# Optimization experiments

Measured on AMD Instinct MI355X. Metric: run time of the kernel, lower is better.

## Reference

```python
import jax, jax.numpy as jnp
import numpy as np

H_SIZE = 1024
N_HEADS = 16
HEAD_DIM = H_SIZE // N_HEADS
TAU2 = 1.0
LN_EPS = 1e-5


def setup_inputs() -> dict:
    key = jax.random.key(0)
    ks = jax.random.split(key, 12)
    B, S = 2, 1024
    s = 1.0 / np.sqrt(H_SIZE)
    inp = {
        "input": jax.random.normal(ks[0], (B, S, H_SIZE), dtype=jnp.float32),
        "input_mask": jnp.ones((B, S), dtype=jnp.float32),
        # uniform(0,1) noise; converted to Gumbel(0,1) inside reference
        "gumbel": jax.random.uniform(ks[1], (B, N_HEADS, S, S), dtype=jnp.float32,
                                     minval=1e-10, maxval=1.0),
        "Wq": jax.random.normal(ks[2], (H_SIZE, H_SIZE), dtype=jnp.float32) * s,
        "bq": jnp.zeros((H_SIZE,), dtype=jnp.float32),
        "Wk": jax.random.normal(ks[3], (H_SIZE, H_SIZE), dtype=jnp.float32) * s,
        "bk": jnp.zeros((H_SIZE,), dtype=jnp.float32),
        "Wv": jax.random.normal(ks[4], (H_SIZE, H_SIZE), dtype=jnp.float32) * s,
        "bv": jnp.zeros((H_SIZE,), dtype=jnp.float32),
        "Wo": jax.random.normal(ks[5], (H_SIZE, H_SIZE), dtype=jnp.float32) * s,
        "bo": jnp.zeros((H_SIZE,), dtype=jnp.float32),
        "gamma": jnp.ones((H_SIZE,), dtype=jnp.float32),
        "beta": jnp.zeros((H_SIZE,), dtype=jnp.float32),
    }
    return inp


def reference(input, input_mask, gumbel, Wq, bq, Wk, bk, Wv, bv, Wo, bo, gamma, beta):
    B, S, _ = input.shape
    # projections -> [B, H, S, D]
    def proj(W, b):
        y = jnp.einsum('bsh,oh->bso', input, W) + b  # torch Linear: x @ W.T + b
        return y.reshape(B, S, N_HEADS, HEAD_DIM).transpose(0, 2, 1, 3)
    qq = proj(Wq, bq)
    kk = proj(Wk, bk)
    vv = proj(Wv, bv)
    # raw scores (NOTE: original has no 1/sqrt(d) scaling)
    interact = jnp.einsum('bhqd,bhkd->bhqk', qq, kk)
    # gumbel-softmax (soft): softmax((logits + g)/tau)
    g = -jnp.log(-jnp.log(gumbel))
    sto_attn = jax.nn.softmax((interact + g) / TAU2, axis=-1)
    # masking: mask_1 over query dim, mask_2 over key dim
    mask = input_mask[:, None, :, None] * input_mask[:, None, None, :]  # [B,1,S,S]
    attn = sto_attn * mask
    # (dropout p=0 -> identity)
    out = jnp.einsum('bhqk,bhkd->bhqd', attn, vv)
    out = out.transpose(0, 2, 1, 3).reshape(B, S, H_SIZE)
    out = jnp.einsum('bsh,oh->bso', out, Wo) + bo
    # residual + layernorm
    x = out + input
    mu = jnp.mean(x, axis=-1, keepdims=True)
    var = jnp.mean(jnp.square(x - mu), axis=-1, keepdims=True)
    return (x - mu) * jax.lax.rsqrt(var + LN_EPS) * gamma + beta
```

## Files before the change

kernel.cpp:

```cpp
#include <hip/hip_runtime.h>

#define S_LEN 1024
#define HSZ   1024
#define NHEAD 16
#define HD    64
#define BATCH 2
#define MROWS 2048
#define SOFTMAX_M0 50.0f

typedef unsigned short u16;
typedef __attribute__((ext_vector_type(8))) short short8;
typedef __attribute__((ext_vector_type(4))) short short4v;
typedef __attribute__((ext_vector_type(4))) float f32x4;

#define MFMA_BF16(a, b, c) __builtin_amdgcn_mfma_f32_16x16x32_bf16((a), (b), (c), 0, 0, 0)

__device__ __forceinline__ u16 f2bf(float f) {
    union { float f; unsigned u; } c; c.f = f;
    unsigned u = c.u;
    u += 0x7fffu + ((u >> 16) & 1u);
    return (u16)(u >> 16);
}
__device__ __forceinline__ float bf2f(u16 s) {
    union { unsigned u; float f; } c; c.u = ((unsigned)s) << 16;
    return c.f;
}
__device__ __forceinline__ short8 ld8(const u16* p) {
    return *reinterpret_cast<const short8*>(p);
}
__device__ __forceinline__ void gld16(const u16* g, u16* l) {
    __builtin_amdgcn_global_load_lds(
        (const __attribute__((address_space(1))) unsigned int*)g,
        (__attribute__((address_space(3))) unsigned int*)l, 16, 0, 0);
}
__device__ __forceinline__ int frag_off(int row, int cbb) {
    return (((row << 3) | (cbb ^ (row & 7))) << 3);
}

template<int MT>
__device__ __forceinline__ void gemm_tile(const u16* __restrict__ Ag,
                                          const u16* __restrict__ Bg,
                                          int klen, u16* As, u16* Bs,
                                          f32x4 (&acc)[MT][4]) {
    const int tid  = threadIdx.x;
    const int wave = tid >> 6, lane = tid & 63;
    const int lr = lane & 15, grp = lane >> 4;
    const int wm = wave >> 1, wn = wave & 1;
    const int ASZ = MT * 2048;
    const int BSZ = 8192;

#pragma unroll
    for (int mt = 0; mt < MT; mt++)
#pragma unroll
        for (int nt = 0; nt < 4; nt++)
            acc[mt][nt] = (f32x4){0.f, 0.f, 0.f, 0.f};

    auto stage = [&](int k0, u16* Ah, u16* Bh) {
#pragma unroll
        for (int j = 0; j < MT; j++) {
            int c = j * 256 + tid, row = c >> 3, cb = (c & 7) ^ (row & 7);
            gld16(Ag + (size_t)row * HSZ + k0 + cb * 8, Ah + c * 8);
        }
#pragma unroll
        for (int j = 0; j < 4; j++) {
            int c = j * 256 + tid, row = c >> 3, cb = (c & 7) ^ (row & 7);
            gld16(Bg + (size_t)row * HSZ + k0 + cb * 8, Bh + c * 8);
        }
    };

    stage(0, As, Bs);

    for (int k0 = 0; k0 < klen; k0 += 64) {
        const int cur = (k0 >> 6) & 1;
        const u16* Ac = As + cur * ASZ;
        const u16* Bc = Bs + cur * BSZ;
        __syncthreads();
        if (k0 + 64 < klen)
            stage(k0 + 64, As + (cur ^ 1) * ASZ, Bs + (cur ^ 1) * BSZ);

#pragma unroll
        for (int h = 0; h < 2; h++) {
            const int cbb = h * 4 + grp;
            short8 af[MT], bf[4];
#pragma unroll
            for (int mt = 0; mt < MT; mt++)
                af[mt] = ld8(Ac + frag_off(wm * (MT * 16) + mt * 16 + lr, cbb));
#pragma unroll
            for (int nt = 0; nt < 4; nt++)
                bf[nt] = ld8(Bc + frag_off(wn * 64 + nt * 16 + lr, cbb));
#pragma unroll
            for (int mt = 0; mt < MT; mt++)
#pragma unroll
                for (int nt = 0; nt < 4; nt++)
                    acc[mt][nt] = MFMA_BF16(af[mt], bf[nt], acc[mt][nt]);
        }
    }
}

__global__ __launch_bounds__(256)
void convert_kernel(const float* __restrict__ x,  const float* __restrict__ wq,
                    const float* __restrict__ wk, const float* __restrict__ wv,
                    const float* __restrict__ wo, u16* __restrict__ dst) {
    const int XV = (MROWS * HSZ) / 4;
    const int WV = (HSZ * HSZ) / 4;
    int vid = blockIdx.x * 256 + threadIdx.x;
    const float* src; int off;
    if (vid < XV)            { src = x;  off = vid; }
    else if (vid < XV + WV)  { src = wq; off = vid - XV; }
    else if (vid < XV + 2*WV){ src = wk; off = vid - XV - WV; }
    else if (vid < XV + 3*WV){ src = wv; off = vid - XV - 2*WV; }
    else                     { src = wo; off = vid - XV - 3*WV; }
    float4 v = reinterpret_cast<const float4*>(src)[off];
    ushort4 o;
    o.x = f2bf(v.x); o.y = f2bf(v.y); o.z = f2bf(v.z); o.w = f2bf(v.w);
    reinterpret_cast<ushort4*>(dst)[vid] = o;
}

__global__ __launch_bounds__(256)
void qkv_gemm(const u16* __restrict__ xb,
              const u16* __restrict__ wqb, const u16* __restrict__ wkb,
              const u16* __restrict__ wvb,
              const float* __restrict__ bq, const float* __restrict__ bk,
              const float* __restrict__ bv, const float* __restrict__ mask,
              u16* __restrict__ qout, u16* __restrict__ kout,
              u16* __restrict__ vtout) {
    __shared__ u16 As[2 * 64 * 64];
    __shared__ u16 Bs[2 * 128 * 64];
    const int ntile = blockIdx.x;
    const int mtile = blockIdx.y;
    const int p  = ntile >> 3;
    const int m0 = mtile * 64;
    const int nw = (ntile & 7) * 128;
    const u16*  W    = (p == 0) ? wqb : (p == 1) ? wkb : wvb;
    const float* bias = (p == 0) ? bq : (p == 1) ? bk : bv;

    f32x4 acc[2][4];
    gemm_tile<2>(xb + (size_t)m0 * HSZ, W + (size_t)nw * HSZ, HSZ, As, Bs, acc);

    const int wave = threadIdx.x >> 6, lane = threadIdx.x & 63;
    const int lr = lane & 15, grp = lane >> 4;
    const int wm = wave >> 1, wn = wave & 1;
#pragma unroll
    for (int mt = 0; mt < 2; mt++)
#pragma unroll
        for (int nt = 0; nt < 4; nt++)
#pragma unroll
            for (int r = 0; r < 4; r++) {
                int m = m0 + wm * 32 + mt * 16 + grp * 4 + r;
                int o = nw + wn * 64 + nt * 16 + lr;
                float val = acc[mt][nt][r] + bias[o];
                int b = m >> 10, s = m & 1023, hh = o >> 6, d = o & 63;
                if (p == 0)
                    qout[(((size_t)(b * NHEAD + hh)) * S_LEN + s) * HD + d] = f2bf(val);
                else if (p == 1)
                    kout[(((size_t)(b * NHEAD + hh)) * S_LEN + s) * HD + d] = f2bf(val);
                else
                    vtout[(((size_t)(b * NHEAD + hh)) * HD + d) * S_LEN + s] =
                        f2bf(val * mask[m]);
            }
}

__global__ __launch_bounds__(256, 4)
void attn_kernel(const u16* __restrict__ qb, const u16* __restrict__ kb,
                 const u16* __restrict__ vt, const float* __restrict__ gumbel,
                 u16* __restrict__ po, float* __restrict__ pl) {
    const int bh   = blockIdx.y;
    const int qt   = blockIdx.x;
    const int half = blockIdx.z;
    const int q0 = qt * 64, kbase = half * 512;
    const int tid = threadIdx.x;
    const int wave = tid >> 6, lane = tid & 63;
    const int lr = lane & 15, grp = lane >> 4;

    const u16* Q = qb + (size_t)bh * S_LEN * HD;
    const u16* K = kb + (size_t)bh * S_LEN * HD;
    const u16* V = vt + (size_t)bh * HD * S_LEN;
    const int qw = q0 + wave * 16;
    const float* Gp = gumbel + (size_t)bh * S_LEN * S_LEN + (size_t)(qw + lr) * S_LEN;

    __shared__ u16 Ks[2][64 * 64];
    __shared__ u16 pbuf[4 * 16 * 68];
    u16* pw = pbuf + wave * (16 * 68);

    short8 aq0 = ld8(Q + (size_t)(qw + lr) * HD + grp * 8);
    short8 aq1 = ld8(Q + (size_t)(qw + lr) * HD + 32 + grp * 8);

    f32x4 acco[4];
#pragma unroll
    for (int i = 0; i < 4; i++) acco[i] = (f32x4){0.f, 0.f, 0.f, 0.f};
    float lsum = 0.f;

    f32x4 gc[4], gn[4];
#pragma unroll
    for (int kt = 0; kt < 4; kt++)
        gc[kt] = *reinterpret_cast<const f32x4*>(Gp + kbase + kt * 16 + grp * 4);

    auto stageK = [&](int k0, u16* Kh) {
#pragma unroll
        for (int j = 0; j < 2; j++) {
            int c = j * 256 + tid, row = c >> 3, cb = (c & 7) ^ (row & 7);
            gld16(K + (size_t)(k0 + row) * HD + cb * 8, Kh + c * 8);
        }
    };
    stageK(kbase, Ks[0]);

#pragma unroll 1
    for (int it = 0; it < 8; it++) {
        const int k0 = kbase + it * 64;
        const int cur = it & 1;

        __syncthreads();
        if (it < 7) {
            stageK(k0 + 64, Ks[cur ^ 1]);
#pragma unroll
            for (int kt = 0; kt < 4; kt++)
                gn[kt] = *reinterpret_cast<const f32x4*>(
                             Gp + k0 + 64 + kt * 16 + grp * 4);
        }

#pragma unroll
        for (int kt = 0; kt < 4; kt++) {
            short8 kf0 = ld8(Ks[cur] + frag_off(kt * 16 + lr, grp));
            short8 kf1 = ld8(Ks[cur] + frag_off(kt * 16 + lr, 4 + grp));
            f32x4 a = (f32x4){0.f, 0.f, 0.f, 0.f};
            a = MFMA_BF16(kf0, aq0, a);
            a = MFMA_BF16(kf1, aq1, a);
            float p[4];
#pragma unroll
            for (int r = 0; r < 4; r++) {
                float w = -__builtin_amdgcn_rcpf(__logf(gc[kt][r]));
                p[r] = __expf(a[r] - SOFTMAX_M0) * w;
                lsum += p[r];
            }
            ushort4 pk;
            pk.x = f2bf(p[0]); pk.y = f2bf(p[1]);
            pk.z = f2bf(p[2]); pk.w = f2bf(p[3]);
            *reinterpret_cast<ushort4*>(pw + lr * 68 + kt * 16 + grp * 4) = pk;
        }

        short8 pa[2];
#pragma unroll
        for (int ks = 0; ks < 2; ks++) {
            const u16* pp = pw + lr * 68 + ks * 32 + grp * 8;
            short4v lo = *reinterpret_cast<const short4v*>(pp);
            short4v hi = *reinterpret_cast<const short4v*>(pp + 4);
            pa[ks] = __builtin_shufflevector(lo, hi, 0, 1, 2, 3, 4, 5, 6, 7);
        }

#pragma unroll
        for (int nt = 0; nt < 4; nt++) {
            const u16* vp = V + (size_t)(nt * 16 + lr) * S_LEN + k0 + grp * 8;
            acco[nt] = MFMA_BF16(pa[0], ld8(vp), acco[nt]);
            acco[nt] = MFMA_BF16(pa[1], ld8(vp + 32), acco[nt]);
        }

        if (it < 7) {
#pragma unroll
            for (int kt = 0; kt < 4; kt++) gc[kt] = gn[kt];
        }
    }

    lsum += __shfl_xor(lsum, 16, 64);
    lsum += __shfl_xor(lsum, 32, 64);

    const int qbase = ((half * 32 + bh) * 16 + qt) * 64 + wave * 16;
    if (lane < 16) pl[qbase + lane] = lsum;

    const int qidx = qbase + grp * 4;
#pragma unroll
    for (int nt = 0; nt < 4; nt++)
#pragma unroll
        for (int r = 0; r < 4; r++)
            po[(size_t)(qidx + r) * 64 + nt * 16 + lr] = f2bf(acco[nt][r]);
}

__global__ __launch_bounds__(256)
void combine_kernel(const u16* __restrict__ po, const float* __restrict__ pl,
                    const float* __restrict__ mask, u16* __restrict__ ctx) {
    const int qt = blockIdx.x, bh = blockIdx.y;
    const int b = bh >> 4, h = bh & 15;
    const int q = threadIdx.x >> 2;
    const int dc = (threadIdx.x & 3) * 16;
    const int i0 = ((0 * 32 + bh) * 16 + qt) * 64 + q;
    const int i1 = ((1 * 32 + bh) * 16 + qt) * 64 + q;
    float l = pl[i0] + pl[i1];
    float mq = mask[b * S_LEN + qt * 64 + q] / l;
    u16* dst = ctx + ((size_t)(b * S_LEN + qt * 64 + q)) * HSZ + h * 64 + dc;
#pragma unroll
    for (int c = 0; c < 2; c++) {
        short8 a = ld8(po + (size_t)i0 * 64 + dc + c * 8);
        short8 bm = ld8(po + (size_t)i1 * 64 + dc + c * 8);
        short8 o;
#pragma unroll
        for (int j = 0; j < 8; j++)
            o[j] = (short)f2bf((bf2f((u16)a[j]) + bf2f((u16)bm[j])) * mq);
        *reinterpret_cast<short8*>(dst + c * 8) = o;
    }
}

__global__ __launch_bounds__(256)
void oproj_gemm(const u16* __restrict__ A, const u16* __restrict__ W,
                float* __restrict__ part0, float* __restrict__ part1) {
    __shared__ u16 As[2 * 64 * 64];
    __shared__ u16 Bs[2 * 128 * 64];
    const int ntile = blockIdx.x;
    const int mtile = blockIdx.y;
    const int z     = blockIdx.z;
    const int m0 = mtile * 64, n0 = ntile * 128, koff = z * 512;

    f32x4 acc[2][4];
    gemm_tile<2>(A + (size_t)m0 * HSZ + koff, W + (size_t)n0 * HSZ + koff,
                 512, As, Bs, acc);

    float* dst = z ? part1 : part0;
    const int wave = threadIdx.x >> 6, lane = threadIdx.x & 63;
    const int lr = lane & 15, grp = lane >> 4;
    const int wm = wave >> 1, wn = wave & 1;
#pragma unroll
    for (int mt = 0; mt < 2; mt++)
#pragma unroll
        for (int nt = 0; nt < 4; nt++)
#pragma unroll
            for (int r = 0; r < 4; r++) {
                int m = m0 + wm * 32 + mt * 16 + grp * 4 + r;
                int o = n0 + wn * 64 + nt * 16 + lr;
                dst[(size_t)m * HSZ + o] = acc[mt][nt][r];
            }
}

__global__ __launch_bounds__(256)
void ln_kernel(const float* __restrict__ part0, const float* __restrict__ part1,
               const float* __restrict__ xin, const float* __restrict__ bo,
               const float* __restrict__ gamma, const float* __restrict__ beta,
               float* __restrict__ out) {
    const int row = blockIdx.x;
    const int tid = threadIdx.x;
    const size_t base = (size_t)row * (HSZ / 4);

    float4 p0 = reinterpret_cast<const float4*>(part0)[base + tid];
    float4 p1 = reinterpret_cast<const float4*>(part1)[base + tid];
    float4 xr = reinterpret_cast<const float4*>(xin)[base + tid];
    float4 bb = reinterpret_cast<const float4*>(bo)[tid];
    float4 v;
    v.x = p0.x + p1.x + xr.x + bb.x;
    v.y = p0.y + p1.y + xr.y + bb.y;
    v.z = p0.z + p1.z + xr.z + bb.z;
    v.w = p0.w + p1.w + xr.w + bb.w;

    float s  = v.x + v.y + v.z + v.w;
    float ss = v.x * v.x + v.y * v.y + v.z * v.z + v.w * v.w;
#pragma unroll
    for (int off = 1; off < 64; off <<= 1) {
        s  += __shfl_xor(s, off, 64);
        ss += __shfl_xor(ss, off, 64);
    }
    __shared__ float red[8];
    int wave = tid >> 6, lane = tid & 63;
    if (lane == 0) { red[wave] = s; red[4 + wave] = ss; }
    __syncthreads();
    s  = red[0] + red[1] + red[2] + red[3];
    ss = red[4] + red[5] + red[6] + red[7];
    float mu  = s * (1.f / HSZ);
    float var = ss * (1.f / HSZ) - mu * mu;
    float rstd = rsqrtf(var + 1e-5f);

    float4 g  = reinterpret_cast<const float4*>(gamma)[tid];
    float4 be = reinterpret_cast<const float4*>(beta)[tid];
    float4 o;
    o.x = (v.x - mu) * rstd * g.x + be.x;
    o.y = (v.y - mu) * rstd * g.y + be.y;
    o.z = (v.z - mu) * rstd * g.z + be.z;
    o.w = (v.w - mu) * rstd * g.w + be.w;
    reinterpret_cast<float4*>(out)[base + tid] = o;
}

extern "C" void kernel_launch(void* const* d_in, const int* in_sizes, int n_in,
                              void* d_out, int out_size, void* d_ws, size_t ws_size,
                              hipStream_t stream) {
    (void)in_sizes; (void)n_in; (void)out_size; (void)ws_size;
    const float* x     = (const float*)d_in[0];
    const float* mask  = (const float*)d_in[1];
    const float* gum   = (const float*)d_in[2];
    const float* Wq    = (const float*)d_in[3];
    const float* bq    = (const float*)d_in[4];
    const float* Wk    = (const float*)d_in[5];
    const float* bk    = (const float*)d_in[6];
    const float* Wv    = (const float*)d_in[7];
    const float* bv    = (const float*)d_in[8];
    const float* Wo    = (const float*)d_in[9];
    const float* bo    = (const float*)d_in[10];
    const float* gamma = (const float*)d_in[11];
    const float* beta  = (const float*)d_in[12];
    float* out = (float*)d_out;

    u16* xb  = (u16*)d_ws;
    u16* wqb = xb  + 2097152;
    u16* wkb = wqb + 1048576;
    u16* wvb = wkb + 1048576;
    u16* wob = wvb + 1048576;
    u16* qb  = wob + 1048576;
    u16* kb  = qb  + 2097152;
    u16* vt  = kb  + 2097152;
    u16* ctx = vt  + 2097152;
    float* part0 = (float*)(ctx + 2097152);
    float* pl    = (float*)((char*)part0 + 8388608);
    u16*   po    = xb;
    float* part1 = (float*)xb;

    convert_kernel<<<dim3(6144), dim3(256), 0, stream>>>(x, Wq, Wk, Wv, Wo, xb);
    qkv_gemm<<<dim3(24, 32), dim3(256), 0, stream>>>(xb, wqb, wkb, wvb,
                                                     bq, bk, bv, mask,
                                                     qb, kb, vt);
    attn_kernel<<<dim3(16, 32, 2), dim3(256), 0, stream>>>(qb, kb, vt, gum, po, pl);
    combine_kernel<<<dim3(16, 32), dim3(256), 0, stream>>>(po, pl, mask, ctx);
    oproj_gemm<<<dim3(8, 32, 2), dim3(256), 0, stream>>>(ctx, wob, part0, part1);
    ln_kernel<<<dim3(2048), dim3(256), 0, stream>>>(part0, part1, x, bo,
                                                    gamma, beta, out);
}
```

Measured before the change: 299.0 us.

## Stage V tiles through LDS with K, swizzle P buffer, nontemporal gumbel loads

V^T tiles are now prefetched into a double-buffered LDS region together with K through async global-to-LDS loads, so the PV MFMAs read swizzled fragments from shared memory instead of issuing direct global loads each iteration. The P scratch buffer drops its padding in favour of an XOR swizzle to avoid bank conflicts. Gumbel noise is read with nontemporal loads so this streamed data does not displace cached lines. LDS use per block roughly doubles, which may reduce occupancy.

After: 293.1 us. 1.02x faster.

```diff
diff --git a/kernel.cpp b/kernel.cpp
--- a/kernel.cpp
+++ b/kernel.cpp
@@ -32,6 +32,9 @@
     __builtin_amdgcn_global_load_lds(
         (const __attribute__((address_space(1))) unsigned int*)g,
         (__attribute__((address_space(3))) unsigned int*)l, 16, 0, 0);
+}
+__device__ __forceinline__ f32x4 ld4_nt(const float* p) {
+    return __builtin_nontemporal_load(reinterpret_cast<const f32x4*>(p));
 }
 __device__ __forceinline__ int frag_off(int row, int cbb) {
     return (((row << 3) | (cbb ^ (row & 7))) << 3);
@@ -179,8 +182,9 @@
     const float* Gp = gumbel + (size_t)bh * S_LEN * S_LEN + (size_t)(qw + lr) * S_LEN;
 
     __shared__ u16 Ks[2][64 * 64];
-    __shared__ u16 pbuf[4 * 16 * 68];
-    u16* pw = pbuf + wave * (16 * 68);
+    __shared__ u16 Vs[2][64 * 64];
+    __shared__ u16 pbuf[4 * 16 * 64];
+    u16* pw = pbuf + wave * (16 * 64);
 
     short8 aq0 = ld8(Q + (size_t)(qw + lr) * HD + grp * 8);
     short8 aq1 = ld8(Q + (size_t)(qw + lr) * HD + 32 + grp * 8);
@@ -193,16 +197,21 @@
     f32x4 gc[4], gn[4];
 #pragma unroll
     for (int kt = 0; kt < 4; kt++)
-        gc[kt] = *reinterpret_cast<const f32x4*>(Gp + kbase + kt * 16 + grp * 4);
-
-    auto stageK = [&](int k0, u16* Kh) {
+        gc[kt] = ld4_nt(Gp + kbase + kt * 16 + grp * 4);
+
+    auto stageKV = [&](int k0, int buf) {
 #pragma unroll
         for (int j = 0; j < 2; j++) {
             int c = j * 256 + tid, row = c >> 3, cb = (c & 7) ^ (row & 7);
-            gld16(K + (size_t)(k0 + row) * HD + cb * 8, Kh + c * 8);
+            gld16(K + (size_t)(k0 + row) * HD + cb * 8, Ks[buf] + c * 8);
+        }
+#pragma unroll
+        for (int j = 0; j < 2; j++) {
+            int c = j * 256 + tid, row = c >> 3, cb = (c & 7) ^ (row & 7);
+            gld16(V + (size_t)row * S_LEN + k0 + cb * 8, Vs[buf] + c * 8);
         }
     };
-    stageK(kbase, Ks[0]);
+    stageKV(kbase, 0);
 
 #pragma unroll 1
     for (int it = 0; it < 8; it++) {
@@ -211,11 +220,10 @@
 
         __syncthreads();
         if (it < 7) {
-            stageK(k0 + 64, Ks[cur ^ 1]);
+            stageKV(k0 + 64, cur ^ 1);
 #pragma unroll
             for (int kt = 0; kt < 4; kt++)
-                gn[kt] = *reinterpret_cast<const f32x4*>(
-                             Gp + k0 + 64 + kt * 16 + grp * 4);
+                gn[kt] = ld4_nt(Gp + k0 + 64 + kt * 16 + grp * 4);
         }
 
 #pragma unroll
@@ -235,24 +243,26 @@
             ushort4 pk;
             pk.x = f2bf(p[0]); pk.y = f2bf(p[1]);
             pk.z = f2bf(p[2]); pk.w = f2bf(p[3]);
-            *reinterpret_cast<ushort4*>(pw + lr * 68 + kt * 16 + grp * 4) = pk;
+            *reinterpret_cast<ushort4*>(
+                pw + lr * 64 + (((kt * 16 + grp * 4) ^ ((lr & 7) << 3)))) = pk;
         }
 
         short8 pa[2];
 #pragma unroll
         for (int ks = 0; ks < 2; ks++) {
-            const u16* pp = pw + lr * 68 + ks * 32 + grp * 8;
+            const u16* pp = pw + lr * 64 + (((ks * 32 + grp * 8) ^ ((lr & 7) << 3)));
             short4v lo = *reinterpret_cast<const short4v*>(pp);
             short4v hi = *reinterpret_cast<const short4v*>(pp + 4);
             pa[ks] = __builtin_shufflevector(lo, hi, 0, 1, 2, 3, 4, 5, 6, 7);
         }
 
 #pragma unroll
-        for (int nt = 0; nt < 4; nt++) {
-            const u16* vp = V + (size_t)(nt * 16 + lr) * S_LEN + k0 + grp * 8;
-            acco[nt] = MFMA_BF16(pa[0], ld8(vp), acco[nt]);
-            acco[nt] = MFMA_BF16(pa[1], ld8(vp + 32), acco[nt]);
-        }
+        for (int nt = 0; nt < 4; nt++)
+#pragma unroll
+            for (int ks = 0; ks < 2; ks++)
+                acco[nt] = MFMA_BF16(pa[ks],
+                                     ld8(Vs[cur] + frag_off(nt * 16 + lr, ks * 4 + grp)),
+                                     acco[nt]);
 
         if (it < 7) {
 #pragma unroll
```

## Widen attention blocks to 128 queries and stage V tiles in LDS

Applied to the files above, without the earlier changes.

Each attention block now handles 128 query rows with 8 waves instead of 64 rows with 4 waves, so every K tile and a newly added shared V tile are loaded once and reused by twice as many waves. V fragments are read from LDS with the swizzled layout instead of directly from global memory. The double-buffered K prefetch is dropped in favour of a load followed by a barrier each iteration, so global load latency is no longer overlapped with compute. The grid is halved to match, and output indexing is remapped so the partial-result layout stays the same.

Result: faster. 290.2 us (-2.9%).

```diff
diff --git a/kernel.cpp b/kernel.cpp
--- a/kernel.cpp
+++ b/kernel.cpp
@@ -160,14 +160,14 @@
             }
 }
 
-__global__ __launch_bounds__(256, 4)
+__global__ __launch_bounds__(512, 4)
 void attn_kernel(const u16* __restrict__ qb, const u16* __restrict__ kb,
                  const u16* __restrict__ vt, const float* __restrict__ gumbel,
                  u16* __restrict__ po, float* __restrict__ pl) {
     const int bh   = blockIdx.y;
-    const int qt   = blockIdx.x;
+    const int qt8  = blockIdx.x;
     const int half = blockIdx.z;
-    const int q0 = qt * 64, kbase = half * 512;
+    const int kbase = half * 512;
     const int tid = threadIdx.x;
     const int wave = tid >> 6, lane = tid & 63;
     const int lr = lane & 15, grp = lane >> 4;
@@ -175,11 +175,12 @@
     const u16* Q = qb + (size_t)bh * S_LEN * HD;
     const u16* K = kb + (size_t)bh * S_LEN * HD;
     const u16* V = vt + (size_t)bh * HD * S_LEN;
-    const int qw = q0 + wave * 16;
+    const int qw = qt8 * 128 + wave * 16;
     const float* Gp = gumbel + (size_t)bh * S_LEN * S_LEN + (size_t)(qw + lr) * S_LEN;
 
-    __shared__ u16 Ks[2][64 * 64];
-    __shared__ u16 pbuf[4 * 16 * 68];
+    __shared__ u16 Ks[64 * 64];
+    __shared__ u16 Vs[64 * 64];
+    __shared__ u16 pbuf[8 * 16 * 68];
     u16* pw = pbuf + wave * (16 * 68);
 
     short8 aq0 = ld8(Q + (size_t)(qw + lr) * HD + grp * 8);
@@ -194,24 +195,23 @@
 #pragma unroll
     for (int kt = 0; kt < 4; kt++)
         gc[kt] = *reinterpret_cast<const f32x4*>(Gp + kbase + kt * 16 + grp * 4);
-
-    auto stageK = [&](int k0, u16* Kh) {
-#pragma unroll
-        for (int j = 0; j < 2; j++) {
-            int c = j * 256 + tid, row = c >> 3, cb = (c & 7) ^ (row & 7);
-            gld16(K + (size_t)(k0 + row) * HD + cb * 8, Kh + c * 8);
-        }
-    };
-    stageK(kbase, Ks[0]);
 
 #pragma unroll 1
     for (int it = 0; it < 8; it++) {
         const int k0 = kbase + it * 64;
-        const int cur = it & 1;
 
         __syncthreads();
+        {
+            int c = tid, row = c >> 3, cb = (c & 7) ^ (row & 7);
+            gld16(K + (size_t)(k0 + row) * HD + cb * 8, Ks + c * 8);
+        }
+        {
+            int c = tid, row = c >> 3, cb = (c & 7) ^ (row & 7);
+            gld16(V + (size_t)row * S_LEN + k0 + cb * 8, Vs + c * 8);
+        }
+        __syncthreads();
+
         if (it < 7) {
-            stageK(k0 + 64, Ks[cur ^ 1]);
 #pragma unroll
             for (int kt = 0; kt < 4; kt++)
                 gn[kt] = *reinterpret_cast<const f32x4*>(
@@ -220,8 +220,8 @@
 
 #pragma unroll
         for (int kt = 0; kt < 4; kt++) {
-            short8 kf0 = ld8(Ks[cur] + frag_off(kt * 16 + lr, grp));
-            short8 kf1 = ld8(Ks[cur] + frag_off(kt * 16 + lr, 4 + grp));
+            short8 kf0 = ld8(Ks + frag_off(kt * 16 + lr, grp));
+            short8 kf1 = ld8(Ks + frag_off(kt * 16 + lr, 4 + grp));
             f32x4 a = (f32x4){0.f, 0.f, 0.f, 0.f};
             a = MFMA_BF16(kf0, aq0, a);
             a = MFMA_BF16(kf1, aq1, a);
@@ -248,11 +248,12 @@
         }
 
 #pragma unroll
-        for (int nt = 0; nt < 4; nt++) {
-            const u16* vp = V + (size_t)(nt * 16 + lr) * S_LEN + k0 + grp * 8;
-            acco[nt] = MFMA_BF16(pa[0], ld8(vp), acco[nt]);
-            acco[nt] = MFMA_BF16(pa[1], ld8(vp + 32), acco[nt]);
-        }
+        for (int nt = 0; nt < 4; nt++)
+#pragma unroll
+            for (int ks = 0; ks < 2; ks++)
+                acco[nt] = MFMA_BF16(pa[ks],
+                                     ld8(Vs + frag_off(nt * 16 + lr, ks * 4 + grp)),
+                                     acco[nt]);
 
         if (it < 7) {
 #pragma unroll
@@ -263,7 +264,8 @@
     lsum += __shfl_xor(lsum, 16, 64);
     lsum += __shfl_xor(lsum, 32, 64);
 
-    const int qbase = ((half * 32 + bh) * 16 + qt) * 64 + wave * 16;
+    const int qbase = ((half * 32 + bh) * 16 + (qt8 * 2 + (wave >> 2))) * 64
+                      + (wave & 3) * 16;
     if (lane < 16) pl[qbase + lane] = lsum;
 
     const int qidx = qbase + grp * 4;
@@ -411,7 +413,7 @@
     qkv_gemm<<<dim3(24, 32), dim3(256), 0, stream>>>(xb, wqb, wkb, wvb,
                                                      bq, bk, bv, mask,
                                                      qb, kb, vt);
-    attn_kernel<<<dim3(16, 32, 2), dim3(256), 0, stream>>>(qb, kb, vt, gum, po, pl);
+    attn_kernel<<<dim3(8, 32, 2), dim3(512), 0, stream>>>(qb, kb, vt, gum, po, pl);
     combine_kernel<<<dim3(16, 32), dim3(256), 0, stream>>>(po, pl, mask, ctx);
     oproj_gemm<<<dim3(8, 32, 2), dim3(256), 0, stream>>>(ctx, wob, part0, part1);
     ln_kernel<<<dim3(2048), dim3(256), 0, stream>>>(part0, part1, x, bo,
```
